# Performance work log

Measured on AMD Instinct MI355X. Metric: run time of the kernel, lower is better.

The kernel has to match this reference:

```python
import math
import jax, jax.numpy as jnp
import numpy as np

FACTOR = 2  # init kwarg of AutoCorrelation


def setup_inputs() -> dict:
    key0 = jax.random.key(0)
    kq, kk, kv = jax.random.split(key0, 3)
    B, H, L, D = 8, 8, 2048, 64
    return {
        "query": jax.random.normal(kq, (B, H, L, D), dtype=jnp.float32),
        "key": jax.random.normal(kk, (B, H, L, D), dtype=jnp.float32),
        "value": jax.random.normal(kv, (B, H, L, D), dtype=jnp.float32),
    }


def reference(query, key, value):
    # Inference (eval-mode) path of AutoCorrelation.forward.
    B, H, L, D = query.shape
    L_KV = key.shape[2]
    # _pad_or_truncate_key_value: match key/value length to query length
    if L > L_KV:
        pad = [(0, 0), (0, 0), (0, L - L_KV), (0, 0)]
        key = jnp.pad(key, pad)
        value = jnp.pad(value, pad)
    else:
        key = key[:, :, :L, :]
        value = value[:, :, :L, :]

    # _period_based_dependency: circular cross-correlation via FFT
    qf = jnp.fft.rfft(jnp.swapaxes(query, -2, -1), axis=-1)   # (B,H,D,L//2+1) complex
    kf = jnp.fft.rfft(jnp.swapaxes(key, -2, -1), axis=-1)
    corr = jnp.fft.irfft(qf * jnp.conj(kf), n=L, axis=-1)     # (B,H,D,L)

    # _time_delay_aggregation (eval branch: per-batch topk delays)
    mean_corr = corr.mean(axis=(1, 2))                         # (B,L)
    num_delays = min(FACTOR * math.ceil(math.log(L)), L)
    w, delay_idx = jax.lax.top_k(mean_corr, num_delays)       # (B,k)
    w = jax.nn.softmax(w, axis=-1)

    ar = jnp.arange(L)

    def body(ctx, inp):
        d, wk = inp  # (B,), (B,)
        idx = (ar[None, :] + d[:, None]) % L                   # (B,L) — circular shift == gather from doubled value
        gathered = jnp.take_along_axis(
            value, jnp.broadcast_to(idx[:, None, :, None], value.shape), axis=2
        )                                                      # (B,H,L,D)
        return ctx + wk[:, None, None, None] * gathered, None

    ctx0 = jnp.zeros_like(value)
    context, _ = jax.lax.scan(body, ctx0, (delay_idx.T, w.T))
    return context
```

## Files before the change

kernel.cpp:

```cpp
#include <hip/hip_runtime.h>

static constexpr int LSEQ = 2048;
static constexpr int NB   = 8;
static constexpr int NH   = 8;
static constexpr int ND   = 64;
static constexpr int NDEL = 16;

static constexpr size_t WS_P_OFF     = 0;
static constexpr size_t WS_W_OFF     = 8388608;
static constexpr size_t WS_DELAY_OFF = 8389120;

__device__ __forceinline__ int SWZ(int x) { return x ^ (((x >> 4) & 7) << 1); }

__device__ __forceinline__ int pof(int f) {
    return ((f & 7) << 8) | (((f >> 3) & 7) << 5) | (((f >> 6) & 7) << 2) | (f >> 9);
}
__device__ __forceinline__ int fofp(int p) {
    return (p >> 8) | (((p >> 5) & 7) << 3) | (((p >> 2) & 7) << 6) | ((p & 3) << 9);
}

#define CMUL(ar, ai, br, bi) make_float2((ar)*(br) - (ai)*(bi), (ar)*(bi) + (ai)*(br))

__device__ __forceinline__ void dft8(const float2 x[8], float2 X[8]) {
    const float RH = 0.70710678118654752440f;
    float2 a0 = make_float2(x[0].x + x[4].x, x[0].y + x[4].y);
    float2 a1 = make_float2(x[1].x + x[5].x, x[1].y + x[5].y);
    float2 a2 = make_float2(x[2].x + x[6].x, x[2].y + x[6].y);
    float2 a3 = make_float2(x[3].x + x[7].x, x[3].y + x[7].y);
    float2 b0 = make_float2(x[0].x - x[4].x, x[0].y - x[4].y);
    float  t1r = x[1].x - x[5].x, t1i = x[1].y - x[5].y;
    float2 b1 = make_float2(RH * (t1r + t1i), RH * (t1i - t1r));
    float  t2r = x[2].x - x[6].x, t2i = x[2].y - x[6].y;
    float2 b2 = make_float2(t2i, -t2r);
    float  t3r = x[3].x - x[7].x, t3i = x[3].y - x[7].y;
    float2 b3 = make_float2(RH * (t3i - t3r), -RH * (t3r + t3i));
    float2 c0 = make_float2(a0.x + a2.x, a0.y + a2.y);
    float2 d0 = make_float2(a0.x - a2.x, a0.y - a2.y);
    float2 c1 = make_float2(a1.x + a3.x, a1.y + a3.y);
    float2 d1 = make_float2(a1.y - a3.y, -(a1.x - a3.x));
    X[0] = make_float2(c0.x + c1.x, c0.y + c1.y);
    X[4] = make_float2(c0.x - c1.x, c0.y - c1.y);
    X[2] = make_float2(d0.x + d1.x, d0.y + d1.y);
    X[6] = make_float2(d0.x - d1.x, d0.y - d1.y);
    float2 e0 = make_float2(b0.x + b2.x, b0.y + b2.y);
    float2 f0 = make_float2(b0.x - b2.x, b0.y - b2.y);
    float2 e1 = make_float2(b1.x + b3.x, b1.y + b3.y);
    float2 f1 = make_float2(b1.y - b3.y, -(b1.x - b3.x));
    X[1] = make_float2(e0.x + e1.x, e0.y + e1.y);
    X[5] = make_float2(e0.x - e1.x, e0.y - e1.y);
    X[3] = make_float2(f0.x + f1.x, f0.y + f1.y);
    X[7] = make_float2(f0.x - f1.x, f0.y - f1.y);
}

__device__ __forceinline__ void dft4(const float2 x[4], float2 X[4]) {
    float2 s0 = make_float2(x[0].x + x[2].x, x[0].y + x[2].y);
    float2 s1 = make_float2(x[1].x + x[3].x, x[1].y + x[3].y);
    float2 d0 = make_float2(x[0].x - x[2].x, x[0].y - x[2].y);
    float2 d1 = make_float2(x[1].y - x[3].y, -(x[1].x - x[3].x));
    X[0] = make_float2(s0.x + s1.x, s0.y + s1.y);
    X[2] = make_float2(s0.x - s1.x, s0.y - s1.y);
    X[1] = make_float2(d0.x + d1.x, d0.y + d1.y);
    X[3] = make_float2(d0.x - d1.x, d0.y - d1.y);
}

__device__ __forceinline__ void stageR8(float2* zp, const int adr[8], const float2 W[7]) {
    float2 X[8], Y[8];
    #pragma unroll
    for (int j = 0; j < 8; ++j) X[j] = zp[adr[j]];
    dft8(X, Y);
    #pragma unroll
    for (int m = 1; m < 8; ++m) Y[m] = CMUL(Y[m].x, Y[m].y, W[m-1].x, W[m-1].y);
    #pragma unroll
    for (int m = 0; m < 8; ++m) zp[adr[m]] = Y[m];
}

__device__ __forceinline__ void stageD(float2* zp, const int adr[8], float2 X[8]) {
    float2 xin[8];
    #pragma unroll
    for (int j = 0; j < 8; ++j) xin[j] = zp[adr[j]];
    dft4(&xin[0], &X[0]);
    dft4(&xin[4], &X[4]);
    #pragma unroll
    for (int m = 0; m < 8; ++m) zp[adr[m]] = X[m];
}

__global__ __launch_bounds__(256, 2) void fft_corr(const float* __restrict__ q,
                                                   const float* __restrict__ k,
                                                   float2* __restrict__ P) {
    __shared__ float2 z0[LSEQ], z1[LSEQ];
    const int t   = threadIdx.x;
    const int bi  = blockIdx.x;
    const int xcd = bi & 7;
    const int sl  = bi >> 3;
    const int bh  = xcd * 8 + (sl >> 3);
    const int grp = sl & 7;
    const int b   = bh >> 3;
    const int h   = bh & 7;
    const size_t base = (size_t)bh * LSEQ * ND + (size_t)(grp * 8);

    float2 WA[7], WB[7], WC[7];
    {
        float sn, cs;
        __sincosf(-6.28318530717958647692f * (float)t / 2048.f, &sn, &cs);
        WA[0] = make_float2(cs, sn);
        __sincosf(-6.28318530717958647692f * (float)(t & 31) / 256.f, &sn, &cs);
        WB[0] = make_float2(cs, sn);
        __sincosf(-6.28318530717958647692f * (float)(t & 3) / 32.f, &sn, &cs);
        WC[0] = make_float2(cs, sn);
        #pragma unroll
        for (int m = 1; m < 7; ++m) {
            WA[m] = CMUL(WA[m-1].x, WA[m-1].y, WA[0].x, WA[0].y);
            WB[m] = CMUL(WB[m-1].x, WB[m-1].y, WB[0].x, WB[0].y);
            WC[m] = CMUL(WC[m-1].x, WC[m-1].y, WC[0].x, WC[0].y);
        }
    }

    int fS[4], pmS[4];
    #pragma unroll
    for (int s = 0; s < 4; ++s) {
        const int cc = (s < 2) ? s : s + 2;
        const int f  = fofp(8 * t + cc);
        const int m  = (2048 - f) & 2047;
        fS[s]  = f;
        pmS[s] = SWZ(pof(m));
    }
    float aFr[4] = {0, 0, 0, 0}, aFi[4] = {0, 0, 0, 0};
    float aS = 0.f;

    const int sbB   = (t >> 5) * 256 + (t & 31);
    const int baseC = (t >> 2) * 32 + (t & 3);
    int adrB[8], adrC[8], adrD[8];
    #pragma unroll
    for (int n = 0; n < 8; ++n) {
        adrB[n] = SWZ(sbB + 32 * n);
        adrC[n] = SWZ(baseC + 4 * n);
        adrD[n] = SWZ(8 * t + n);
    }

    #pragma unroll
    for (int half = 0; half < 2; ++half) {
        float4 qa[8], ka[8];
        #pragma unroll
        for (int j = 0; j < 8; ++j) {
            const size_t r = base + (size_t)(t + 256 * j) * ND + half * 4;
            qa[j] = *(const float4*)(q + r);
            ka[j] = *(const float4*)(k + r);
        }
        #pragma unroll
        for (int pr = 0; pr < 2; ++pr) {
            const int c0 = 2 * pr, c1 = 2 * pr + 1;
            float2 X0[8], X1[8], Y0[8], Y1[8];
            #pragma unroll
            for (int j = 0; j < 8; ++j) {
                X0[j] = make_float2((&qa[j].x)[c0], (&ka[j].x)[c0]);
                X1[j] = make_float2((&qa[j].x)[c1], (&ka[j].x)[c1]);
            }
            __syncthreads();

            dft8(X0, Y0);
            dft8(X1, Y1);
            #pragma unroll
            for (int m = 1; m < 8; ++m) {
                Y0[m] = CMUL(Y0[m].x, Y0[m].y, WA[m-1].x, WA[m-1].y);
                Y1[m] = CMUL(Y1[m].x, Y1[m].y, WA[m-1].x, WA[m-1].y);
            }
            #pragma unroll
            for (int m = 0; m < 8; ++m) {
                const int a = SWZ(m * 256 + t);
                z0[a] = Y0[m];
                z1[a] = Y1[m];
            }
            __syncthreads();

            stageR8(z0, adrB, WB);
            stageR8(z1, adrB, WB);
            __syncthreads();

            stageR8(z0, adrC, WC);
            stageR8(z1, adrC, WC);
            __syncthreads();

            stageD(z0, adrD, X0);
            stageD(z1, adrD, X1);
            __syncthreads();

            #pragma unroll
            for (int s = 0; s < 4; ++s) {
                const int cc = (s < 2) ? s : s + 2;
                {
                    const float2 Zf = X0[cc], Zm = z0[pmS[s]];
                    const float qr = 0.5f * (Zf.x + Zm.x), qi = 0.5f * (Zf.y - Zm.y);
                    const float kr = 0.5f * (Zf.y + Zm.y), ki = 0.5f * (Zm.x - Zf.x);
                    aFr[s] += qr * kr + qi * ki;
                    aFi[s] += qi * kr - qr * ki;
                }
                {
                    const float2 Zf = X1[cc], Zm = z1[pmS[s]];
                    const float qr = 0.5f * (Zf.x + Zm.x), qi = 0.5f * (Zf.y - Zm.y);
                    const float kr = 0.5f * (Zf.y + Zm.y), ki = 0.5f * (Zm.x - Zf.x);
                    aFr[s] += qr * kr + qi * ki;
                    aFi[s] += qi * kr - qr * ki;
                }
            }
            if (t == 0) aS += X0[2].x * X0[2].y + X1[2].x * X1[2].y;
        }
    }

    const int part = h * 8 + grp;
    float2* Pp = P + (size_t)part * (NB * 2048) + (size_t)b * 2048;
    *(float4*)&Pp[8 * t]     = make_float4(aFr[0], aFi[0], aFr[1], aFi[1]);
    *(float4*)&Pp[8 * t + 4] = make_float4(aFr[2], aFi[2], aFr[3], aFi[3]);
    #pragma unroll
    for (int s = 0; s < 4; ++s) {
        const int m = (2048 - fS[s]) & 2047;
        if (m != fS[s]) Pp[pof(m)] = make_float2(aFr[s], -aFi[s]);
    }
    if (t == 0) Pp[pof(1024)] = make_float2(aS, 0.f);
}

__global__ __launch_bounds__(256) void reduce_S(float2* __restrict__ P) {
    const int g = blockIdx.x * 256 + threadIdx.x;
    float ax = 0.f, ay = 0.f;
    #pragma unroll 8
    for (int part = 0; part < 64; ++part) {
        const float2 v = P[(size_t)part * (NB * 2048) + g];
        ax += v.x; ay += v.y;
    }
    P[g] = make_float2(ax, ay);
}

__global__ __launch_bounds__(256) void ifft_topk(const float2* __restrict__ S,
                                                 float* __restrict__ wout,
                                                 int* __restrict__ dout) {
    __shared__ float2 zz[LSEQ];
    __shared__ float  mc[LSEQ];
    __shared__ float  pv[4];
    __shared__ int    pig[4];
    __shared__ float  topv[NDEL];
    __shared__ int    topi[NDEL];
    const int b = blockIdx.x, t = threadIdx.x;

    float2 WA[7], WB[7], WC[7];
    {
        float sn, cs;
        __sincosf(-6.28318530717958647692f * (float)t / 2048.f, &sn, &cs);
        WA[0] = make_float2(cs, sn);
        __sincosf(-6.28318530717958647692f * (float)(t & 31) / 256.f, &sn, &cs);
        WB[0] = make_float2(cs, sn);
        __sincosf(-6.28318530717958647692f * (float)(t & 3) / 32.f, &sn, &cs);
        WC[0] = make_float2(cs, sn);
        #pragma unroll
        for (int m = 1; m < 7; ++m) {
            WA[m] = CMUL(WA[m-1].x, WA[m-1].y, WA[0].x, WA[0].y);
            WB[m] = CMUL(WB[m-1].x, WB[m-1].y, WB[0].x, WB[0].y);
            WC[m] = CMUL(WC[m-1].x, WC[m-1].y, WC[0].x, WC[0].y);
        }
    }
    const int sbB   = (t >> 5) * 256 + (t & 31);
    const int baseC = (t >> 2) * 32 + (t & 3);
    int adrB[8], adrC[8], adrD[8];
    #pragma unroll
    for (int n = 0; n < 8; ++n) {
        adrB[n] = SWZ(sbB + 32 * n);
        adrC[n] = SWZ(baseC + 4 * n);
        adrD[n] = SWZ(8 * t + n);
    }

    #pragma unroll
    for (int j = 0; j < 8; ++j) zz[t + 256 * j] = S[b * 2048 + t + 256 * j];
    __syncthreads();

    float2 X[8], Y[8];
    #pragma unroll
    for (int j = 0; j < 8; ++j) {
        const float2 s = zz[pof(t + 256 * j)];
        X[j] = make_float2(s.x, -s.y);
    }
    __syncthreads();

    dft8(X, Y);
    #pragma unroll
    for (int m = 1; m < 8; ++m) Y[m] = CMUL(Y[m].x, Y[m].y, WA[m-1].x, WA[m-1].y);
    #pragma unroll
    for (int m = 0; m < 8; ++m) zz[SWZ(m * 256 + t)] = Y[m];
    __syncthreads();

    stageR8(zz, adrB, WB);
    __syncthreads();
    stageR8(zz, adrC, WC);
    __syncthreads();

    {
        float2 xin[8];
        #pragma unroll
        for (int j = 0; j < 8; ++j) xin[j] = zz[adrD[j]];
        dft4(&xin[0], &X[0]);
        dft4(&xin[4], &X[4]);
    }

    const float scale = 1.0f / ((float)LSEQ * (float)(NH * ND));
    #pragma unroll
    for (int cc = 0; cc < 8; ++cc) mc[fofp(8 * t + cc)] = X[cc].x * scale;
    __syncthreads();

    const int lane = t & 63, wv = t >> 6;
    for (int it = 0; it < NDEL; ++it) {
        float bv = -3e38f; int bix = 0;
        #pragma unroll
        for (int u = 0; u < 8; ++u) {
            const int idx = t + 256 * u;
            const float v = mc[idx];
            if (v > bv || (v == bv && idx < bix)) { bv = v; bix = idx; }
        }
        #pragma unroll
        for (int off = 32; off; off >>= 1) {
            const float ov = __shfl_xor(bv, off);
            const int   oi = __shfl_xor(bix, off);
            if (ov > bv || (ov == bv && oi < bix)) { bv = ov; bix = oi; }
        }
        if (lane == 0) { pv[wv] = bv; pig[wv] = bix; }
        __syncthreads();
        if (t < 64) {
            float v = (t < 4) ? pv[t] : -3e38f;
            int  ii = (t < 4) ? pig[t] : 0;
            #pragma unroll
            for (int off = 2; off; off >>= 1) {
                const float ov = __shfl_xor(v, off);
                const int   oi = __shfl_xor(ii, off);
                if (ov > v || (ov == v && oi < ii)) { v = ov; ii = oi; }
            }
            if (t == 0) { topv[it] = v; topi[it] = ii; mc[ii] = -3e38f; }
        }
        __syncthreads();
    }

    if (t == 0) {
        const float m = topv[0];
        float e[NDEL], sum = 0.f;
        for (int i = 0; i < NDEL; ++i) { e[i] = __expf(topv[i] - m); sum += e[i]; }
        const float inv = 1.0f / sum;
        for (int i = 0; i < NDEL; ++i) {
            wout[b * NDEL + i] = e[i] * inv;
            dout[b * NDEL + i] = topi[i];
        }
    }
}

__global__ __launch_bounds__(256) void gather_out(const float* __restrict__ v,
                                                  const float* __restrict__ w,
                                                  const int* __restrict__ delay,
                                                  float* __restrict__ out) {
    const int bi  = blockIdx.x;
    const int xcd = bi & 7;
    const int s   = bi >> 3;
    const int bh  = xcd * 8 + (s >> 7);
    const int bt  = s & 127;
    const int b   = bh >> 3;
    const int tid = threadIdx.x;

    __shared__ float sw_[NDEL];
    __shared__ int   sd_[NDEL];
    if (tid < NDEL) {
        sw_[tid] = w[b * NDEL + tid];
        sd_[tid] = delay[b * NDEL + tid];
    }
    __syncthreads();

    const float* vb = v + (size_t)bh * LSEQ * ND;
    float*       ob = out + (size_t)bh * LSEQ * ND;

    const int row = tid >> 4;
    const int col = (tid & 15) * 4;
    const int t   = bt * 16 + row;

    float4 acc = make_float4(0.f, 0.f, 0.f, 0.f);
    #pragma unroll
    for (int kk = 0; kk < NDEL; ++kk) {
        const int r = (t + sd_[kk]) & (LSEQ - 1);
        const float4 vv = *(const float4*)(vb + (size_t)r * ND + col);
        const float wv = sw_[kk];
        acc.x += wv * vv.x; acc.y += wv * vv.y;
        acc.z += wv * vv.z; acc.w += wv * vv.w;
    }
    *(float4*)(ob + (size_t)t * ND + col) = acc;
}

extern "C" void kernel_launch(void* const* d_in, const int* in_sizes, int n_in,
                              void* d_out, int out_size, void* d_ws, size_t ws_size,
                              hipStream_t stream) {
    const float* q = (const float*)d_in[0];
    const float* k = (const float*)d_in[1];
    const float* v = (const float*)d_in[2];
    float* out = (float*)d_out;

    float2* P     = (float2*)((char*)d_ws + WS_P_OFF);
    float*  w     = (float*)((char*)d_ws + WS_W_OFF);
    int*    delay = (int*)((char*)d_ws + WS_DELAY_OFF);

    fft_corr<<<dim3(512), dim3(256), 0, stream>>>(q, k, P);
    reduce_S<<<dim3(64), dim3(256), 0, stream>>>(P);
    ifft_topk<<<dim3(NB), dim3(256), 0, stream>>>(P, w, delay);
    gather_out<<<dim3(NB * NH * 128), dim3(256), 0, stream>>>(v, w, delay, out);
}
```

Measured before the change: 202.5 us.

## Split FFT correlation blocks by column half and reduce partials with atomics

Each fft_corr block now handles one 4-column half instead of looping over both halves. This doubles the grid to 1024 blocks and raises the launch-bounds occupancy hint to 4. The per-part partial spectrum buffer and the separate reduce_S kernel are replaced by float atomicAdd into a small buffer that a new zero_S kernel clears first. The aim is more parallelism, better latency hiding and one less kernel pass over the partials, at the cost of heavy atomic contention, with 128 contributors per element, and non-deterministic summation order.

```diff
diff --git a/kernel.cpp b/kernel.cpp
--- a/kernel.cpp
+++ b/kernel.cpp
@@ -84,19 +84,23 @@
     for (int m = 0; m < 8; ++m) zp[adr[m]] = X[m];
 }
 
-__global__ __launch_bounds__(256, 2) void fft_corr(const float* __restrict__ q,
+__global__ __launch_bounds__(256) void zero_S(float4* __restrict__ P4) {
+    P4[blockIdx.x * 256 + threadIdx.x] = make_float4(0.f, 0.f, 0.f, 0.f);
+}
+
+__global__ __launch_bounds__(256, 4) void fft_corr(const float* __restrict__ q,
                                                    const float* __restrict__ k,
                                                    float2* __restrict__ P) {
     __shared__ float2 z0[LSEQ], z1[LSEQ];
-    const int t   = threadIdx.x;
-    const int bi  = blockIdx.x;
-    const int xcd = bi & 7;
-    const int sl  = bi >> 3;
-    const int bh  = xcd * 8 + (sl >> 3);
-    const int grp = sl & 7;
-    const int b   = bh >> 3;
-    const int h   = bh & 7;
-    const size_t base = (size_t)bh * LSEQ * ND + (size_t)(grp * 8);
+    const int t    = threadIdx.x;
+    const int bi   = blockIdx.x;
+    const int xcd  = bi & 7;
+    const int sl   = bi >> 3;
+    const int bh   = xcd * 8 + (sl >> 4);
+    const int grp  = (sl >> 1) & 7;
+    const int half = sl & 1;
+    const int b    = bh >> 3;
+    const size_t base = (size_t)bh * LSEQ * ND + (size_t)(grp * 8 + half * 4);
 
     float2 WA[7], WB[7], WC[7];
     {
@@ -137,96 +141,87 @@
         adrD[n] = SWZ(8 * t + n);
     }
 
-    #pragma unroll
-    for (int half = 0; half < 2; ++half) {
-        float4 qa[8], ka[8];
+    float4 qa[8], ka[8];
+    #pragma unroll
+    for (int j = 0; j < 8; ++j) {
+        const size_t r = base + (size_t)(t + 256 * j) * ND;
+        qa[j] = *(const float4*)(q + r);
+        ka[j] = *(const float4*)(k + r);
+    }
+    #pragma unroll
+    for (int pr = 0; pr < 2; ++pr) {
+        const int c0 = 2 * pr, c1 = 2 * pr + 1;
+        float2 X0[8], X1[8], Y0[8], Y1[8];
         #pragma unroll
         for (int j = 0; j < 8; ++j) {
-            const size_t r = base + (size_t)(t + 256 * j) * ND + half * 4;
-            qa[j] = *(const float4*)(q + r);
-            ka[j] = *(const float4*)(k + r);
-        }
-        #pragma unroll
-        for (int pr = 0; pr < 2; ++pr) {
-            const int c0 = 2 * pr, c1 = 2 * pr + 1;
-            float2 X0[8], X1[8], Y0[8], Y1[8];
-            #pragma unroll
-            for (int j = 0; j < 8; ++j) {
-                X0[j] = make_float2((&qa[j].x)[c0], (&ka[j].x)[c0]);
-                X1[j] = make_float2((&qa[j].x)[c1], (&ka[j].x)[c1]);
+            X0[j] = make_float2((&qa[j].x)[c0], (&ka[j].x)[c0]);
+            X1[j] = make_float2((&qa[j].x)[c1], (&ka[j].x)[c1]);
+        }
+        __syncthreads();
+
+        dft8(X0, Y0);
+        dft8(X1, Y1);
+        #pragma unroll
+        for (int m = 1; m < 8; ++m) {
+            Y0[m] = CMUL(Y0[m].x, Y0[m].y, WA[m-1].x, WA[m-1].y);
+            Y1[m] = CMUL(Y1[m].x, Y1[m].y, WA[m-1].x, WA[m-1].y);
+        }
+        #pragma unroll
+        for (int m = 0; m < 8; ++m) {
+            const int a = SWZ(m * 256 + t);
+            z0[a] = Y0[m];
+            z1[a] = Y1[m];
+        }
+        __syncthreads();
+
+        stageR8(z0, adrB, WB);
+        stageR8(z1, adrB, WB);
+        __syncthreads();
+
+        stageR8(z0, adrC, WC);
+        stageR8(z1, adrC, WC);
+        __syncthreads();
+
+        stageD(z0, adrD, X0);
+        stageD(z1, adrD, X1);
+        __syncthreads();
+
+        #pragma unroll
+        for (int s = 0; s < 4; ++s) {
+            const int cc = (s < 2) ? s : s + 2;
+            {
+                const float2 Zf = X0[cc], Zm = z0[pmS[s]];
+                const float qr = 0.5f * (Zf.x + Zm.x), qi = 0.5f * (Zf.y - Zm.y);
+                const float kr = 0.5f * (Zf.y + Zm.y), ki = 0.5f * (Zm.x - Zf.x);
+                aFr[s] += qr * kr + qi * ki;
+                aFi[s] += qi * kr - qr * ki;
             }
-            __syncthreads();
-
-            dft8(X0, Y0);
-            dft8(X1, Y1);
-            #pragma unroll
-            for (int m = 1; m < 8; ++m) {
-                Y0[m] = CMUL(Y0[m].x, Y0[m].y, WA[m-1].x, WA[m-1].y);
-                Y1[m] = CMUL(Y1[m].x, Y1[m].y, WA[m-1].x, WA[m-1].y);
+            {
+                const float2 Zf = X1[cc], Zm = z1[pmS[s]];
+                const float qr = 0.5f * (Zf.x + Zm.x), qi = 0.5f * (Zf.y - Zm.y);
+                const float kr = 0.5f * (Zf.y + Zm.y), ki = 0.5f * (Zm.x - Zf.x);
+                aFr[s] += qr * kr + qi * ki;
+                aFi[s] += qi * kr - qr * ki;
             }
-            #pragma unroll
-            for (int m = 0; m < 8; ++m) {
-                const int a = SWZ(m * 256 + t);
-                z0[a] = Y0[m];
-                z1[a] = Y1[m];
-            }
-            __syncthreads();
-
-            stageR8(z0, adrB, WB);
-            stageR8(z1, adrB, WB);
-            __syncthreads();
-
-            stageR8(z0, adrC, WC);
-            stageR8(z1, adrC, WC);
-            __syncthreads();
-
-            stageD(z0, adrD, X0);
-            stageD(z1, adrD, X1);
-            __syncthreads();
-
-            #pragma unroll
-            for (int s = 0; s < 4; ++s) {
-                const int cc = (s < 2) ? s : s + 2;
-                {
-                    const float2 Zf = X0[cc], Zm = z0[pmS[s]];
-                    const float qr = 0.5f * (Zf.x + Zm.x), qi = 0.5f * (Zf.y - Zm.y);
-                    const float kr = 0.5f * (Zf.y + Zm.y), ki = 0.5f * (Zm.x - Zf.x);
-                    aFr[s] += qr * kr + qi * ki;
-                    aFi[s] += qi * kr - qr * ki;
-                }
-                {
-                    const float2 Zf = X1[cc], Zm = z1[pmS[s]];
-                    const float qr = 0.5f * (Zf.x + Zm.x), qi = 0.5f * (Zf.y - Zm.y);
-                    const float kr = 0.5f * (Zf.y + Zm.y), ki = 0.5f * (Zm.x - Zf.x);
-                    aFr[s] += qr * kr + qi * ki;
-                    aFi[s] += qi * kr - qr * ki;
-                }
-            }
-            if (t == 0) aS += X0[2].x * X0[2].y + X1[2].x * X1[2].y;
-        }
-    }
-
-    const int part = h * 8 + grp;
-    float2* Pp = P + (size_t)part * (NB * 2048) + (size_t)b * 2048;
-    *(float4*)&Pp[8 * t]     = make_float4(aFr[0], aFi[0], aFr[1], aFi[1]);
-    *(float4*)&Pp[8 * t + 4] = make_float4(aFr[2], aFi[2], aFr[3], aFi[3]);
+        }
+        if (t == 0) aS += X0[2].x * X0[2].y + X1[2].x * X1[2].y;
+    }
+
+    float2* Pp = P + (size_t)b * 2048;
     #pragma unroll
     for (int s = 0; s < 4; ++s) {
+        const int cc = (s < 2) ? s : s + 2;
+        float* pd = (float*)(Pp + (8 * t + cc));
+        atomicAdd(pd,     aFr[s]);
+        atomicAdd(pd + 1, aFi[s]);
         const int m = (2048 - fS[s]) & 2047;
-        if (m != fS[s]) Pp[pof(m)] = make_float2(aFr[s], -aFi[s]);
-    }
-    if (t == 0) Pp[pof(1024)] = make_float2(aS, 0.f);
-}
-
-__global__ __launch_bounds__(256) void reduce_S(float2* __restrict__ P) {
-    const int g = blockIdx.x * 256 + threadIdx.x;
-    float ax = 0.f, ay = 0.f;
-    #pragma unroll 8
-    for (int part = 0; part < 64; ++part) {
-        const float2 v = P[(size_t)part * (NB * 2048) + g];
-        ax += v.x; ay += v.y;
-    }
-    P[g] = make_float2(ax, ay);
+        if (m != fS[s]) {
+            float* pm = (float*)(Pp + pof(m));
+            atomicAdd(pm,     aFr[s]);
+            atomicAdd(pm + 1, -aFi[s]);
+        }
+    }
+    if (t == 0) atomicAdd((float*)(Pp + 2 ), aS);
 }
 
 __global__ __launch_bounds__(256) void ifft_topk(const float2* __restrict__ S,
@@ -397,8 +392,8 @@
     float*  w     = (float*)((char*)d_ws + WS_W_OFF);
     int*    delay = (int*)((char*)d_ws + WS_DELAY_OFF);
 
-    fft_corr<<<dim3(512), dim3(256), 0, stream>>>(q, k, P);
-    reduce_S<<<dim3(64), dim3(256), 0, stream>>>(P);
+    zero_S<<<dim3(32), dim3(256), 0, stream>>>((float4*)P);
+    fft_corr<<<dim3(1024), dim3(256), 0, stream>>>(q, k, P);
     ifft_topk<<<dim3(NB), dim3(256), 0, stream>>>(P, w, delay);
     gather_out<<<dim3(NB * NH * 128), dim3(256), 0, stream>>>(v, w, delay, out);
 }
```

Measured after the change: 416.6 us. +105.7%, slower.

## Split fft_corr column halves across two 256-thread groups with shared reduction

Applied to the files above, without the earlier changes.

fft_corr now launches 512 threads per block. Each 256-thread half processes one of the two 4-column halves concurrently, using its own pair of shared-memory FFT buffers, where before one 256-thread block handled both halves one after the other. The two halves' spectral accumulators are combined through shared memory before the single write to P. This doubles per-block parallelism and shortens each block's serial chain, at the cost of twice the LDS per block (64KB), which may limit how many blocks fit per CU.

```diff
diff --git a/kernel.cpp b/kernel.cpp
--- a/kernel.cpp
+++ b/kernel.cpp
@@ -84,11 +84,13 @@
     for (int m = 0; m < 8; ++m) zp[adr[m]] = X[m];
 }
 
-__global__ __launch_bounds__(256, 2) void fft_corr(const float* __restrict__ q,
+__global__ __launch_bounds__(512, 4) void fft_corr(const float* __restrict__ q,
                                                    const float* __restrict__ k,
                                                    float2* __restrict__ P) {
-    __shared__ float2 z0[LSEQ], z1[LSEQ];
+    __shared__ float2 z[4][LSEQ];
     const int t   = threadIdx.x;
+    const int tl  = t & 255;
+    const int hf  = t >> 8;
     const int bi  = blockIdx.x;
     const int xcd = bi & 7;
     const int sl  = bi >> 3;
@@ -96,16 +98,19 @@
     const int grp = sl & 7;
     const int b   = bh >> 3;
     const int h   = bh & 7;
-    const size_t base = (size_t)bh * LSEQ * ND + (size_t)(grp * 8);
+    const size_t base = (size_t)bh * LSEQ * ND + (size_t)(grp * 8 + hf * 4);
+
+    float2* const p0 = z[2 * hf];
+    float2* const p1 = z[2 * hf + 1];
 
     float2 WA[7], WB[7], WC[7];
     {
         float sn, cs;
-        __sincosf(-6.28318530717958647692f * (float)t / 2048.f, &sn, &cs);
+        __sincosf(-6.28318530717958647692f * (float)tl / 2048.f, &sn, &cs);
         WA[0] = make_float2(cs, sn);
-        __sincosf(-6.28318530717958647692f * (float)(t & 31) / 256.f, &sn, &cs);
+        __sincosf(-6.28318530717958647692f * (float)(tl & 31) / 256.f, &sn, &cs);
         WB[0] = make_float2(cs, sn);
-        __sincosf(-6.28318530717958647692f * (float)(t & 3) / 32.f, &sn, &cs);
+        __sincosf(-6.28318530717958647692f * (float)(tl & 3) / 32.f, &sn, &cs);
         WC[0] = make_float2(cs, sn);
         #pragma unroll
         for (int m = 1; m < 7; ++m) {
@@ -119,7 +124,7 @@
     #pragma unroll
     for (int s = 0; s < 4; ++s) {
         const int cc = (s < 2) ? s : s + 2;
-        const int f  = fofp(8 * t + cc);
+        const int f  = fofp(8 * tl + cc);
         const int m  = (2048 - f) & 2047;
         fS[s]  = f;
         pmS[s] = SWZ(pof(m));
@@ -127,95 +132,108 @@
     float aFr[4] = {0, 0, 0, 0}, aFi[4] = {0, 0, 0, 0};
     float aS = 0.f;
 
-    const int sbB   = (t >> 5) * 256 + (t & 31);
-    const int baseC = (t >> 2) * 32 + (t & 3);
+    const int sbB   = (tl >> 5) * 256 + (tl & 31);
+    const int baseC = (tl >> 2) * 32 + (tl & 3);
     int adrB[8], adrC[8], adrD[8];
     #pragma unroll
     for (int n = 0; n < 8; ++n) {
         adrB[n] = SWZ(sbB + 32 * n);
         adrC[n] = SWZ(baseC + 4 * n);
-        adrD[n] = SWZ(8 * t + n);
-    }
-
-    #pragma unroll
-    for (int half = 0; half < 2; ++half) {
-        float4 qa[8], ka[8];
+        adrD[n] = SWZ(8 * tl + n);
+    }
+
+    float4 qa[8], ka[8];
+    #pragma unroll
+    for (int j = 0; j < 8; ++j) {
+        const size_t r = base + (size_t)(tl + 256 * j) * ND;
+        qa[j] = *(const float4*)(q + r);
+        ka[j] = *(const float4*)(k + r);
+    }
+    #pragma unroll
+    for (int pr = 0; pr < 2; ++pr) {
+        const int c0 = 2 * pr, c1 = 2 * pr + 1;
+        float2 X0[8], X1[8], Y0[8], Y1[8];
         #pragma unroll
         for (int j = 0; j < 8; ++j) {
-            const size_t r = base + (size_t)(t + 256 * j) * ND + half * 4;
-            qa[j] = *(const float4*)(q + r);
-            ka[j] = *(const float4*)(k + r);
-        }
-        #pragma unroll
-        for (int pr = 0; pr < 2; ++pr) {
-            const int c0 = 2 * pr, c1 = 2 * pr + 1;
-            float2 X0[8], X1[8], Y0[8], Y1[8];
-            #pragma unroll
-            for (int j = 0; j < 8; ++j) {
-                X0[j] = make_float2((&qa[j].x)[c0], (&ka[j].x)[c0]);
-                X1[j] = make_float2((&qa[j].x)[c1], (&ka[j].x)[c1]);
+            X0[j] = make_float2((&qa[j].x)[c0], (&ka[j].x)[c0]);
+            X1[j] = make_float2((&qa[j].x)[c1], (&ka[j].x)[c1]);
+        }
+        __syncthreads();
+
+        dft8(X0, Y0);
+        dft8(X1, Y1);
+        #pragma unroll
+        for (int m = 1; m < 8; ++m) {
+            Y0[m] = CMUL(Y0[m].x, Y0[m].y, WA[m-1].x, WA[m-1].y);
+            Y1[m] = CMUL(Y1[m].x, Y1[m].y, WA[m-1].x, WA[m-1].y);
+        }
+        #pragma unroll
+        for (int m = 0; m < 8; ++m) {
+            const int a = SWZ(m * 256 + tl);
+            p0[a] = Y0[m];
+            p1[a] = Y1[m];
+        }
+        __syncthreads();
+
+        stageR8(p0, adrB, WB);
+        stageR8(p1, adrB, WB);
+        __syncthreads();
+
+        stageR8(p0, adrC, WC);
+        stageR8(p1, adrC, WC);
+        __syncthreads();
+
+        stageD(p0, adrD, X0);
+        stageD(p1, adrD, X1);
+        __syncthreads();
+
+        #pragma unroll
+        for (int s = 0; s < 4; ++s) {
+            const int cc = (s < 2) ? s : s + 2;
+            {
+                const float2 Zf = X0[cc], Zm = p0[pmS[s]];
+                const float qr = 0.5f * (Zf.x + Zm.x), qi = 0.5f * (Zf.y - Zm.y);
+                const float kr = 0.5f * (Zf.y + Zm.y), ki = 0.5f * (Zm.x - Zf.x);
+                aFr[s] += qr * kr + qi * ki;
+                aFi[s] += qi * kr - qr * ki;
             }
-            __syncthreads();
-
-            dft8(X0, Y0);
-            dft8(X1, Y1);
-            #pragma unroll
-            for (int m = 1; m < 8; ++m) {
-                Y0[m] = CMUL(Y0[m].x, Y0[m].y, WA[m-1].x, WA[m-1].y);
-                Y1[m] = CMUL(Y1[m].x, Y1[m].y, WA[m-1].x, WA[m-1].y);
+            {
+                const float2 Zf = X1[cc], Zm = p1[pmS[s]];
+                const float qr = 0.5f * (Zf.x + Zm.x), qi = 0.5f * (Zf.y - Zm.y);
+                const float kr = 0.5f * (Zf.y + Zm.y), ki = 0.5f * (Zm.x - Zf.x);
+                aFr[s] += qr * kr + qi * ki;
+                aFi[s] += qi * kr - qr * ki;
             }
-            #pragma unroll
-            for (int m = 0; m < 8; ++m) {
-                const int a = SWZ(m * 256 + t);
-                z0[a] = Y0[m];
-                z1[a] = Y1[m];
-            }
-            __syncthreads();
-
-            stageR8(z0, adrB, WB);
-            stageR8(z1, adrB, WB);
-            __syncthreads();
-
-            stageR8(z0, adrC, WC);
-            stageR8(z1, adrC, WC);
-            __syncthreads();
-
-            stageD(z0, adrD, X0);
-            stageD(z1, adrD, X1);
-            __syncthreads();
-
-            #pragma unroll
-            for (int s = 0; s < 4; ++s) {
-                const int cc = (s < 2) ? s : s + 2;
-                {
-                    const float2 Zf = X0[cc], Zm = z0[pmS[s]];
-                    const float qr = 0.5f * (Zf.x + Zm.x), qi = 0.5f * (Zf.y - Zm.y);
-                    const float kr = 0.5f * (Zf.y + Zm.y), ki = 0.5f * (Zm.x - Zf.x);
-                    aFr[s] += qr * kr + qi * ki;
-                    aFi[s] += qi * kr - qr * ki;
-                }
-                {
-                    const float2 Zf = X1[cc], Zm = z1[pmS[s]];
-                    const float qr = 0.5f * (Zf.x + Zm.x), qi = 0.5f * (Zf.y - Zm.y);
-                    const float kr = 0.5f * (Zf.y + Zm.y), ki = 0.5f * (Zm.x - Zf.x);
-                    aFr[s] += qr * kr + qi * ki;
-                    aFi[s] += qi * kr - qr * ki;
-                }
-            }
-            if (t == 0) aS += X0[2].x * X0[2].y + X1[2].x * X1[2].y;
-        }
-    }
-
-    const int part = h * 8 + grp;
-    float2* Pp = P + (size_t)part * (NB * 2048) + (size_t)b * 2048;
-    *(float4*)&Pp[8 * t]     = make_float4(aFr[0], aFi[0], aFr[1], aFi[1]);
-    *(float4*)&Pp[8 * t + 4] = make_float4(aFr[2], aFi[2], aFr[3], aFi[3]);
-    #pragma unroll
-    for (int s = 0; s < 4; ++s) {
-        const int m = (2048 - fS[s]) & 2047;
-        if (m != fS[s]) Pp[pof(m)] = make_float2(aFr[s], -aFi[s]);
-    }
-    if (t == 0) Pp[pof(1024)] = make_float2(aS, 0.f);
+        }
+        if (tl == 0) aS += X0[2].x * X0[2].y + X1[2].x * X1[2].y;
+    }
+
+    __syncthreads();
+    float4* const rb4 = (float4*)&z[0][0];
+    float*  const rbS = (float*)&z[1][0];
+    if (hf == 1) {
+        rb4[2 * tl]     = make_float4(aFr[0], aFi[0], aFr[1], aFi[1]);
+        rb4[2 * tl + 1] = make_float4(aFr[2], aFi[2], aFr[3], aFi[3]);
+        if (tl == 0) rbS[0] = aS;
+    }
+    __syncthreads();
+    if (hf == 0) {
+        const float4 r0 = rb4[2 * tl], r1 = rb4[2 * tl + 1];
+        aFr[0] += r0.x; aFi[0] += r0.y; aFr[1] += r0.z; aFi[1] += r0.w;
+        aFr[2] += r1.x; aFi[2] += r1.y; aFr[3] += r1.z; aFi[3] += r1.w;
+        if (tl == 0) aS += rbS[0];
+
+        const int part = h * 8 + grp;
+        float2* Pp = P + (size_t)part * (NB * 2048) + (size_t)b * 2048;
+        *(float4*)&Pp[8 * tl]     = make_float4(aFr[0], aFi[0], aFr[1], aFi[1]);
+        *(float4*)&Pp[8 * tl + 4] = make_float4(aFr[2], aFi[2], aFr[3], aFi[3]);
+        #pragma unroll
+        for (int s = 0; s < 4; ++s) {
+            const int m = (2048 - fS[s]) & 2047;
+            if (m != fS[s]) Pp[pof(m)] = make_float2(aFr[s], -aFi[s]);
+        }
+        if (tl == 0) Pp[pof(1024)] = make_float2(aS, 0.f);
+    }
 }
 
 __global__ __launch_bounds__(256) void reduce_S(float2* __restrict__ P) {
@@ -397,7 +415,7 @@
     float*  w     = (float*)((char*)d_ws + WS_W_OFF);
     int*    delay = (int*)((char*)d_ws + WS_DELAY_OFF);
 
-    fft_corr<<<dim3(512), dim3(256), 0, stream>>>(q, k, P);
+    fft_corr<<<dim3(512), dim3(512), 0, stream>>>(q, k, P);
     reduce_S<<<dim3(64), dim3(256), 0, stream>>>(P);
     ifft_topk<<<dim3(NB), dim3(256), 0, stream>>>(P, w, delay);
     gather_out<<<dim3(NB * NH * 128), dim3(256), 0, stream>>>(v, w, delay, out);
```

Result: slower. 232.0 us (+14.6%).
